# Kernel optimization log

Hardware: AMD Instinct MI355X
Metric: run time of the kernel (lower is better)

The kernel has to match this reference:

```python
import jax, jax.numpy as jnp
import numpy as np

M, K, N = 8192, 4096, 4096


def setup_inputs() -> dict:
    key = jax.random.key(0)
    k1, k2, k3, k4 = jax.random.split(key, 4)
    x = jax.random.normal(k1, (M, K), dtype=jnp.float32)
    # int8 weight buffer (qweight), per-output-channel dequant scales, bf16-style bias
    weight_q = jax.random.randint(k2, (N, K), -128, 128, dtype=jnp.int32).astype(jnp.int8)
    qscales = jax.random.uniform(k3, (N,), dtype=jnp.float32) * 0.01 + 0.005
    bias = jax.random.normal(k4, (N,), dtype=jnp.float32) * 0.01
    return {"x": x, "weight_q": weight_q, "qscales": qscales, "bias": bias}


def reference(x, weight_q, qscales, bias):
    # dynamic per-tensor activation quantization: clampv = max(x)
    clampv = jnp.max(x)
    x8 = jnp.clip(jnp.round(x * (127.0 / clampv)), -128, 127).astype(jnp.int8)
    acc = jax.lax.dot_general(
        x8, weight_q,
        dimension_numbers=(((1,), (1,)), ((), ())),
        preferred_element_type=jnp.int32,
    )
    # fused dequant: (acc*alpha + bias/qscales)*qscales == acc*alpha*qscales + bias
    out = acc.astype(jnp.float32) * (clampv / 127.0) * qscales[None, :] + bias[None, :]
    return out
```

## Files before the change

### kernel.cpp

```cpp
#include <hip/hip_runtime.h>
#include <math.h>

#define MDIM 8192
#define KDIM 4096
#define NDIM 4096

typedef int v4i __attribute__((ext_vector_type(4)));

__device__ __forceinline__ void gload_lds16(const void* g, void* l) {
  __builtin_amdgcn_global_load_lds(
      (const __attribute__((address_space(1))) void*)g,
      (__attribute__((address_space(3))) void*)l,
      16, 0, 0);
}

__device__ __forceinline__ float key_to_float(unsigned key) {
  unsigned b = (key & 0x80000000u) ? (key & 0x7FFFFFFFu) : ~key;
  return __uint_as_float(b);
}

constexpr int PACK_B = 768, MAX_B = 1280;

__global__ void __launch_bounds__(256) kprep(const int* __restrict__ w,
                                             signed char* __restrict__ w8,
                                             const float* __restrict__ x,
                                             unsigned int* __restrict__ key_out) {
  if (blockIdx.x < PACK_B) {
    __shared__ int smode;
    int ok = 1;
    #pragma unroll
    for (int i = 0; i < 16; ++i) {
      int v = w[threadIdx.x * 16 + i];
      ok &= (v >= -128) & (v <= 127);
    }
    if (threadIdx.x == 0) smode = 1;
    __syncthreads();
    if (!ok) atomicAnd(&smode, 0);
    __syncthreads();
    const int mode = smode;

    const int n16 = NDIM * KDIM / 16;
    int tid = blockIdx.x * blockDim.x + threadIdx.x;
    int stride = PACK_B * blockDim.x;
    int4* dst = (int4*)w8;
    if (mode) {
      const int4* src = (const int4*)w;
      for (int i = tid; i < n16; i += stride) {
        int4 r;
        #pragma unroll
        for (int q = 0; q < 4; ++q) {
          int4 a = src[(size_t)i * 4 + q];
          int packed = (a.x & 255) | ((a.y & 255) << 8) |
                       ((a.z & 255) << 16) | ((a.w & 255) << 24);
          ((int*)&r)[q] = packed;
        }
        dst[i] = r;
      }
    } else {
      const int4* src = (const int4*)w;
      for (int i = tid; i < n16; i += stride) dst[i] = src[i];
    }
  } else {
    const int n4 = MDIM * KDIM / 4;
    int b = blockIdx.x - PACK_B;
    int tid = b * blockDim.x + threadIdx.x;
    int stride = MAX_B * blockDim.x;
    float m = -3.4e38f;
    const float4* x4 = (const float4*)x;
    for (int i = tid; i < n4; i += stride) {
      float4 v = x4[i];
      m = fmaxf(m, fmaxf(fmaxf(v.x, v.y), fmaxf(v.z, v.w)));
    }
    #pragma unroll
    for (int off = 32; off > 0; off >>= 1)
      m = fmaxf(m, __shfl_down(m, off, 64));
    __shared__ float sm[4];
    int lane = threadIdx.x & 63, wv = threadIdx.x >> 6;
    if (lane == 0) sm[wv] = m;
    __syncthreads();
    if (threadIdx.x == 0) {
      m = fmaxf(fmaxf(sm[0], sm[1]), fmaxf(sm[2], sm[3]));
      unsigned bb = __float_as_uint(m);
      unsigned key = (bb & 0x80000000u) ? ~bb : (bb | 0x80000000u);
      atomicMax(key_out, key);
    }
  }
}

__device__ __forceinline__ int pack4(float4 v, float s) {
  int q0 = (int)fminf(fmaxf(rintf(v.x * s), -128.f), 127.f);
  int q1 = (int)fminf(fmaxf(rintf(v.y * s), -128.f), 127.f);
  int q2 = (int)fminf(fmaxf(rintf(v.z * s), -128.f), 127.f);
  int q3 = (int)fminf(fmaxf(rintf(v.w * s), -128.f), 127.f);
  return (q0 & 255) | ((q1 & 255) << 8) | ((q2 & 255) << 16) | ((q3 & 255) << 24);
}

__global__ void __launch_bounds__(256) kquant(const float* __restrict__ x,
                                              signed char* __restrict__ x8,
                                              const unsigned* __restrict__ keyp) {
  float s = 127.0f / key_to_float(*keyp);
  const int n16 = MDIM * KDIM / 16;
  int tid = blockIdx.x * blockDim.x + threadIdx.x;
  int stride = gridDim.x * blockDim.x;
  const float4* x4 = (const float4*)x;
  int4* out16 = (int4*)x8;
  for (int i = tid; i < n16; i += stride) {
    const float4* src = x4 + (size_t)i * 4;
    int4 r;
    r.x = pack4(src[0], s);
    r.y = pack4(src[1], s);
    r.z = pack4(src[2], s);
    r.w = pack4(src[3], s);
    out16[i] = r;
  }
}

constexpr int BM = 256, BN = 256, BK = 128;
constexpr int NT = KDIM / BK;

__device__ __forceinline__ v4i mfma_i8(v4i a, v4i b, v4i c) {
  return __builtin_amdgcn_mfma_i32_16x16x64_i8(a, b, c, 0, 0, 0);
}

__global__ void __launch_bounds__(512, 2) kgemm(
    const signed char* __restrict__ A8,
    const signed char* __restrict__ W8,
    const float* __restrict__ qs,
    const float* __restrict__ bias,
    const unsigned* __restrict__ keyp,
    float* __restrict__ out) {
  __shared__ alignas(1024) signed char lds[2][2][2][128 * 128];

  const int nbn = NDIM / BN;
  const int nwg = (MDIM / BM) * nbn;
  int bid = blockIdx.x;
  int wg = (bid & 7) * (nwg / 8) + (bid >> 3);
  const int brow = (wg / nbn) * BM;
  const int bcol = (wg % nbn) * BN;

  const int tid = threadIdx.x;
  const int lane = tid & 63;
  const int wv = tid >> 6;
  const int wr = wv >> 2, wc = wv & 3;
  const int lhi = lane >> 4, llo = lane & 15;

  const signed char* Abase = A8 + (size_t)brow * KDIM;
  const signed char* Bbase = W8 + (size_t)bcol * KDIM;

  auto stageA = [&](int t, int h) {
    signed char* dst = &lds[t & 1][0][h][0];
    const size_t k0 = (size_t)t * BK;
    #pragma unroll
    for (int l = 0; l < 2; ++l) {
      int p = l * 512 + tid;
      int r = p >> 3, s = p & 7;
      int R = ((r >> 6) << 7) + h * 64 + (r & 63);
      int g = s ^ (r & 7);
      gload_lds16(Abase + (size_t)R * KDIM + k0 + g * 16, dst + p * 16);
    }
  };
  auto stageB = [&](int t, int h) {
    signed char* dst = &lds[t & 1][1][h][0];
    const size_t k0 = (size_t)t * BK;
    #pragma unroll
    for (int l = 0; l < 2; ++l) {
      int p = l * 512 + tid;
      int r = p >> 3, s = p & 7;
      int R = ((r >> 5) << 6) + h * 32 + (r & 31);
      int g = s ^ (r & 7);
      gload_lds16(Bbase + (size_t)R * KDIM + k0 + g * 16, dst + p * 16);
    }
  };
  auto readA = [&](int par, int mi, int ks) -> v4i {
    int h = mi >> 2;
    int r = wr * 64 + (mi & 3) * 16 + llo;
    int s = (ks * 4 + lhi) ^ (llo & 7);
    return *(const v4i*)&lds[par][0][h][r * 128 + s * 16];
  };
  auto readB = [&](int par, int ni, int ks) -> v4i {
    int h = ni >> 1;
    int r = wc * 32 + (ni & 1) * 16 + llo;
    int s = (ks * 4 + lhi) ^ (llo & 7);
    return *(const v4i*)&lds[par][1][h][r * 128 + s * 16];
  };

  v4i acc[8][4];
  v4i zero = {0, 0, 0, 0};
  #pragma unroll
  for (int i = 0; i < 8; ++i)
    #pragma unroll
    for (int j = 0; j < 4; ++j) acc[i][j] = zero;

  stageA(0, 0); stageA(0, 1); stageB(0, 0); stageB(0, 1);
  asm volatile("s_waitcnt vmcnt(0)" ::: "memory");
  __builtin_amdgcn_s_barrier();

  #pragma unroll 2
  for (int t = 0; t < NT; ++t) {
    const int par = t & 1;
    v4i afr[8][2], bfr[4][2];

    if (t + 1 < NT) {
      stageA(t + 1, 0); stageA(t + 1, 1);
      stageB(t + 1, 0); stageB(t + 1, 1);
    }
    __builtin_amdgcn_sched_barrier(0);

    #pragma unroll
    for (int ni = 0; ni < 2; ++ni) {
      bfr[ni][0] = readB(par, ni, 0);
      bfr[ni][1] = readB(par, ni, 1);
    }
    #pragma unroll
    for (int mi = 0; mi < 4; ++mi) {
      afr[mi][0] = readA(par, mi, 0);
      afr[mi][1] = readA(par, mi, 1);
    }
    #pragma unroll
    for (int ni = 2; ni < 4; ++ni) {
      bfr[ni][0] = readB(par, ni, 0);
      bfr[ni][1] = readB(par, ni, 1);
    }
    #pragma unroll
    for (int mi = 4; mi < 8; ++mi) {
      afr[mi][0] = readA(par, mi, 0);
      afr[mi][1] = readA(par, mi, 1);
    }

    #pragma unroll
    for (int mi = 0; mi < 8; ++mi)
      #pragma unroll
      for (int ni = 0; ni < 4; ++ni) {
        acc[mi][ni] = mfma_i8(afr[mi][0], bfr[ni][0], acc[mi][ni]);
        acc[mi][ni] = mfma_i8(afr[mi][1], bfr[ni][1], acc[mi][ni]);
      }

    asm volatile("s_waitcnt vmcnt(0)" ::: "memory");
    __builtin_amdgcn_s_barrier();
  }

  const float alpha = key_to_float(*keyp) * (1.0f / 127.0f);
  #pragma unroll
  for (int ni = 0; ni < 4; ++ni) {
    int n = bcol + wc * 64 + ni * 16 + llo;
    float sc = qs[n] * alpha;
    float bv = bias[n];
    #pragma unroll
    for (int mi = 0; mi < 8; ++mi) {
      int m0 = brow + wr * 128 + mi * 16 + lhi * 4;
      #pragma unroll
      for (int j = 0; j < 4; ++j)
        out[(size_t)(m0 + j) * NDIM + n] = (float)acc[mi][ni][j] * sc + bv;
    }
  }
}

extern "C" void kernel_launch(void* const* d_in, const int* in_sizes, int n_in,
                              void* d_out, int out_size, void* d_ws, size_t ws_size,
                              hipStream_t stream) {
  const float* x = (const float*)d_in[0];
  const int* wq = (const int*)d_in[1];
  const float* qscales = (const float*)d_in[2];
  const float* bias = (const float*)d_in[3];
  float* out = (float*)d_out;

  unsigned* keyp = (unsigned*)d_ws;
  signed char* x8 = (signed char*)d_ws + 256;
  signed char* w8 = x8 + (size_t)MDIM * KDIM;

  (void)hipMemsetAsync(keyp, 0, 4, stream);
  kprep<<<PACK_B + MAX_B, 256, 0, stream>>>(wq, w8, x, keyp);
  kquant<<<2048, 256, 0, stream>>>(x, x8, keyp);
  kgemm<<<(MDIM / BM) * (NDIM / BN), 512, 0, stream>>>(x8, w8, qscales, bias, keyp, out);
}
```

Before: 204.2 us.

## Use 1024-thread GEMM blocks with 64x64 per-wave tiles and unified LDS staging

The int8 GEMM block grows from 8 to 16 waves while the 256x256 output tile stays the same. Each wave now computes a 64x64 sub-tile instead of 128x64. The split half-tile LDS layout becomes one contiguous 256-row buffer per operand, and each thread issues half as many staging loads. The intent is more waves per CU to hide memory and LDS latency. In exchange each wave reuses its fragments less, so LDS read traffic rises, and the (1024,4) launch bound may squeeze the register budget enough to cause spills.

New measurement: 241.5 us. +18.3%, slower.

```diff
diff --git a/kernel.cpp b/kernel.cpp
--- a/kernel.cpp
+++ b/kernel.cpp
@@ -122,14 +122,14 @@
   return __builtin_amdgcn_mfma_i32_16x16x64_i8(a, b, c, 0, 0, 0);
 }
 
-__global__ void __launch_bounds__(512, 2) kgemm(
+__global__ void __launch_bounds__(1024, 4) kgemm(
     const signed char* __restrict__ A8,
     const signed char* __restrict__ W8,
     const float* __restrict__ qs,
     const float* __restrict__ bias,
     const unsigned* __restrict__ keyp,
     float* __restrict__ out) {
-  __shared__ alignas(1024) signed char lds[2][2][2][128 * 128];
+  __shared__ alignas(1024) signed char lds[2][2][256 * 128];
 
   const int nbn = NDIM / BN;
   const int nwg = (MDIM / BM) * nbn;
@@ -147,67 +147,60 @@
   const signed char* Abase = A8 + (size_t)brow * KDIM;
   const signed char* Bbase = W8 + (size_t)bcol * KDIM;
 
-  auto stageA = [&](int t, int h) {
-    signed char* dst = &lds[t & 1][0][h][0];
+  auto stageA = [&](int t) {
+    signed char* dst = &lds[t & 1][0][0];
     const size_t k0 = (size_t)t * BK;
     #pragma unroll
     for (int l = 0; l < 2; ++l) {
-      int p = l * 512 + tid;
+      int p = l * 1024 + tid;
       int r = p >> 3, s = p & 7;
-      int R = ((r >> 6) << 7) + h * 64 + (r & 63);
       int g = s ^ (r & 7);
-      gload_lds16(Abase + (size_t)R * KDIM + k0 + g * 16, dst + p * 16);
-    }
-  };
-  auto stageB = [&](int t, int h) {
-    signed char* dst = &lds[t & 1][1][h][0];
+      gload_lds16(Abase + (size_t)r * KDIM + k0 + g * 16, dst + p * 16);
+    }
+  };
+  auto stageB = [&](int t) {
+    signed char* dst = &lds[t & 1][1][0];
     const size_t k0 = (size_t)t * BK;
     #pragma unroll
     for (int l = 0; l < 2; ++l) {
-      int p = l * 512 + tid;
+      int p = l * 1024 + tid;
       int r = p >> 3, s = p & 7;
-      int R = ((r >> 5) << 6) + h * 32 + (r & 31);
       int g = s ^ (r & 7);
-      gload_lds16(Bbase + (size_t)R * KDIM + k0 + g * 16, dst + p * 16);
+      gload_lds16(Bbase + (size_t)r * KDIM + k0 + g * 16, dst + p * 16);
     }
   };
   auto readA = [&](int par, int mi, int ks) -> v4i {
-    int h = mi >> 2;
-    int r = wr * 64 + (mi & 3) * 16 + llo;
+    int r = wr * 64 + mi * 16 + llo;
     int s = (ks * 4 + lhi) ^ (llo & 7);
-    return *(const v4i*)&lds[par][0][h][r * 128 + s * 16];
+    return *(const v4i*)&lds[par][0][r * 128 + s * 16];
   };
   auto readB = [&](int par, int ni, int ks) -> v4i {
-    int h = ni >> 1;
-    int r = wc * 32 + (ni & 1) * 16 + llo;
+    int r = wc * 64 + ni * 16 + llo;
     int s = (ks * 4 + lhi) ^ (llo & 7);
-    return *(const v4i*)&lds[par][1][h][r * 128 + s * 16];
-  };
-
-  v4i acc[8][4];
+    return *(const v4i*)&lds[par][1][r * 128 + s * 16];
+  };
+
+  v4i acc[4][4];
   v4i zero = {0, 0, 0, 0};
   #pragma unroll
-  for (int i = 0; i < 8; ++i)
+  for (int i = 0; i < 4; ++i)
     #pragma unroll
     for (int j = 0; j < 4; ++j) acc[i][j] = zero;
 
-  stageA(0, 0); stageA(0, 1); stageB(0, 0); stageB(0, 1);
+  stageA(0); stageB(0);
   asm volatile("s_waitcnt vmcnt(0)" ::: "memory");
   __builtin_amdgcn_s_barrier();
 
   #pragma unroll 2
   for (int t = 0; t < NT; ++t) {
     const int par = t & 1;
-    v4i afr[8][2], bfr[4][2];
-
-    if (t + 1 < NT) {
-      stageA(t + 1, 0); stageA(t + 1, 1);
-      stageB(t + 1, 0); stageB(t + 1, 1);
-    }
+    v4i afr[4][2], bfr[4][2];
+
+    if (t + 1 < NT) { stageA(t + 1); stageB(t + 1); }
     __builtin_amdgcn_sched_barrier(0);
 
     #pragma unroll
-    for (int ni = 0; ni < 2; ++ni) {
+    for (int ni = 0; ni < 4; ++ni) {
       bfr[ni][0] = readB(par, ni, 0);
       bfr[ni][1] = readB(par, ni, 1);
     }
@@ -216,19 +209,9 @@
       afr[mi][0] = readA(par, mi, 0);
       afr[mi][1] = readA(par, mi, 1);
     }
-    #pragma unroll
-    for (int ni = 2; ni < 4; ++ni) {
-      bfr[ni][0] = readB(par, ni, 0);
-      bfr[ni][1] = readB(par, ni, 1);
-    }
-    #pragma unroll
-    for (int mi = 4; mi < 8; ++mi) {
-      afr[mi][0] = readA(par, mi, 0);
-      afr[mi][1] = readA(par, mi, 1);
-    }
-
-    #pragma unroll
-    for (int mi = 0; mi < 8; ++mi)
+
+    #pragma unroll
+    for (int mi = 0; mi < 4; ++mi)
       #pragma unroll
       for (int ni = 0; ni < 4; ++ni) {
         acc[mi][ni] = mfma_i8(afr[mi][0], bfr[ni][0], acc[mi][ni]);
@@ -246,8 +229,8 @@
     float sc = qs[n] * alpha;
     float bv = bias[n];
     #pragma unroll
-    for (int mi = 0; mi < 8; ++mi) {
-      int m0 = brow + wr * 128 + mi * 16 + lhi * 4;
+    for (int mi = 0; mi < 4; ++mi) {
+      int m0 = brow + wr * 64 + mi * 16 + lhi * 4;
       #pragma unroll
       for (int j = 0; j < 4; ++j)
         out[(size_t)(m0 + j) * NDIM + n] = (float)acc[mi][ni][j] * sc + bv;
@@ -271,5 +254,5 @@
   (void)hipMemsetAsync(keyp, 0, 4, stream);
   kprep<<<PACK_B + MAX_B, 256, 0, stream>>>(wq, w8, x, keyp);
   kquant<<<2048, 256, 0, stream>>>(x, x8, keyp);
-  kgemm<<<(MDIM / BM) * (NDIM / BN), 512, 0, stream>>>(x8, w8, qscales, bias, keyp, out);
-}
+  kgemm<<<(MDIM / BM) * (NDIM / BN), 1024, 0, stream>>>(x8, w8, qscales, bias, keyp, out);
+}
```

## Defer last MFMA quadrant to next iteration to overlap with LDS reads

Applied to the files above, without the earlier changes.

The MFMAs for the lower-right quadrant of each wave's tile (mi 4-7, ni 2-3) are moved into the next iteration. They run there from fragments kept in registers, ahead of that iteration's LDS fragment reads, and a tail loop after the main loop finishes the last ones. The aim is to keep the matrix units busy while the LDS reads are in flight, hiding read latency across the barrier. Holding the extra 12 v4i fragments raises VGPR pressure at 2 waves/SIMD, which risks spills.

New measurement: 202.6 us. Within noise of the previous version (-0.8%).

```diff
diff --git a/kernel.cpp b/kernel.cpp
--- a/kernel.cpp
+++ b/kernel.cpp
@@ -191,6 +191,8 @@
     #pragma unroll
     for (int j = 0; j < 4; ++j) acc[i][j] = zero;
 
+  v4i dA[4][2], dB[2][2];
+
   stageA(0, 0); stageA(0, 1); stageB(0, 0); stageB(0, 1);
   asm volatile("s_waitcnt vmcnt(0)" ::: "memory");
   __builtin_amdgcn_s_barrier();
@@ -206,6 +208,16 @@
     }
     __builtin_amdgcn_sched_barrier(0);
 
+    if (t > 0) {
+      #pragma unroll
+      for (int mi = 0; mi < 4; ++mi)
+        #pragma unroll
+        for (int ni = 0; ni < 2; ++ni) {
+          acc[4 + mi][2 + ni] = mfma_i8(dA[mi][0], dB[ni][0], acc[4 + mi][2 + ni]);
+          acc[4 + mi][2 + ni] = mfma_i8(dA[mi][1], dB[ni][1], acc[4 + mi][2 + ni]);
+        }
+    }
+
     #pragma unroll
     for (int ni = 0; ni < 2; ++ni) {
       bfr[ni][0] = readB(par, ni, 0);
@@ -228,16 +240,41 @@
     }
 
     #pragma unroll
-    for (int mi = 0; mi < 8; ++mi)
+    for (int mi = 0; mi < 4; ++mi)
       #pragma unroll
       for (int ni = 0; ni < 4; ++ni) {
         acc[mi][ni] = mfma_i8(afr[mi][0], bfr[ni][0], acc[mi][ni]);
         acc[mi][ni] = mfma_i8(afr[mi][1], bfr[ni][1], acc[mi][ni]);
       }
+    #pragma unroll
+    for (int mi = 4; mi < 8; ++mi)
+      #pragma unroll
+      for (int ni = 0; ni < 2; ++ni) {
+        acc[mi][ni] = mfma_i8(afr[mi][0], bfr[ni][0], acc[mi][ni]);
+        acc[mi][ni] = mfma_i8(afr[mi][1], bfr[ni][1], acc[mi][ni]);
+      }
+    #pragma unroll
+    for (int mi = 0; mi < 4; ++mi) {
+      dA[mi][0] = afr[4 + mi][0];
+      dA[mi][1] = afr[4 + mi][1];
+    }
+    #pragma unroll
+    for (int ni = 0; ni < 2; ++ni) {
+      dB[ni][0] = bfr[2 + ni][0];
+      dB[ni][1] = bfr[2 + ni][1];
+    }
 
     asm volatile("s_waitcnt vmcnt(0)" ::: "memory");
     __builtin_amdgcn_s_barrier();
   }
+
+  #pragma unroll
+  for (int mi = 0; mi < 4; ++mi)
+    #pragma unroll
+    for (int ni = 0; ni < 2; ++ni) {
+      acc[4 + mi][2 + ni] = mfma_i8(dA[mi][0], dB[ni][0], acc[4 + mi][2 + ni]);
+      acc[4 + mi][2 + ni] = mfma_i8(dA[mi][1], dB[ni][1], acc[4 + mi][2 + ni]);
+    }
 
   const float alpha = key_to_float(*keyp) * (1.0f / 127.0f);
   #pragma unroll
```
